# Kernel tuning notes

Hardware: AMD Instinct MI355X
Metric: run time of the kernel (lower is better)

Reference implementation:

```python
import jax, jax.numpy as jnp
import numpy as np

N, E, B = 10000, 160000, 16
IN, H, A, L, OUT = 16, 64, 8, 2, 1
MSG_IN = 2 * (H + 1) + 1   # 131 = concat(x_i, x_j, additional_message_features)
UPD_IN = H + 1 + H         # 129 = concat(x_aug, aggregated message)


def _tp(h, a, W, b):
    # scalar-irreps fully-connected O3 tensor product == bilinear map + bias
    return jnp.einsum('ni,nj,ijk->nk', h, a, W) + b


def setup_inputs() -> dict:
    key = jax.random.key(0)
    ks = jax.random.split(key, 24)
    f32 = jnp.float32
    def rn(k, shape, scale=1.0):
        return jax.random.normal(k, shape, f32) * scale
    def w(k, shape):
        fan = shape[-3] * shape[-2]
        return rn(k, shape, 1.0 / np.sqrt(fan))
    return {
        'x': rn(ks[0], (N, IN)),
        'edge_index': jax.random.randint(ks[1], (2, E), 0, N),
        'edge_attr': rn(ks[2], (E, A)),
        'node_attr': rn(ks[3], (N, A)),
        'additional_message_features': rn(ks[4], (E, 1)),
        'additional_node_features': rn(ks[5], (N, 1)),
        'batch': jnp.sort(jax.random.randint(ks[6], (N,), 0, B)),
        'W_emb': w(ks[7], (IN + 1, A, H)), 'b_emb': jnp.zeros((H,), f32),
        'Wm1': w(ks[8], (L, MSG_IN, A, H)), 'bm1': jnp.zeros((L, H), f32),
        'Wm2': w(ks[9], (L, H, A, H)), 'bm2': jnp.zeros((L, H), f32),
        'Wu1': w(ks[10], (L, UPD_IN, A, H)), 'bu1': jnp.zeros((L, H), f32),
        'Wu2': w(ks[11], (L, H, A, H)), 'bu2': jnp.zeros((L, H), f32),
        'Wp1': w(ks[12], (H, A, H)), 'bp1': jnp.zeros((H,), f32),
        'Wp2': w(ks[13], (H, A, H)), 'bp2': jnp.zeros((H,), f32),
        'Wq1': rn(ks[14], (H, H), 1.0 / np.sqrt(H)), 'bq1': jnp.zeros((H,), f32),
        'Wq2': rn(ks[15], (H, OUT), 1.0 / np.sqrt(H)), 'bq2': jnp.zeros((OUT,), f32),
    }


def _forward(x, edge_attr, node_attr, amf, anf,
             W_emb, b_emb, Wm1, bm1, Wm2, bm2, Wu1, bu1, Wu2, bu2,
             Wp1, bp1, Wp2, bp2, Wq1, bq1, Wq2, bq2, edge_index, batch):
    silu = jax.nn.silu
    src, dst = edge_index[0], edge_index[1]  # source_to_target: aggregate at dst
    n = x.shape[0]
    # embedding: concat additional node features, bilinear TP with node_attr
    h = _tp(jnp.concatenate([x, anf], -1), node_attr, W_emb, b_emb)          # [N,H]
    for l in range(Wm1.shape[0]):  # loop over structurally distinct layers
        h_aug = jnp.concatenate([h, anf], -1)                                # [N,H+1]
        m_in = jnp.concatenate([h_aug[dst], h_aug[src], amf], -1)            # [E,MSG_IN]
        m = silu(_tp(m_in, edge_attr, Wm1[l], bm1[l]))                       # TP + swish gate
        m = silu(_tp(m, edge_attr, Wm2[l], bm2[l]))                          # sg2=True -> gated too
        agg = jax.ops.segment_sum(m, dst, num_segments=n)                    # scatter-add [N,H]
        u = silu(_tp(jnp.concatenate([h_aug, agg], -1), node_attr, Wu1[l], bu1[l]))
        u = _tp(u, node_attr, Wu2[l], bu2[l])                                # no gate on 2nd TP
        h = h + u                                                            # residual, adnid stripped
    # pre-pool MLP (SwishGate TP then plain TP)
    p = silu(_tp(h, node_attr, Wp1, bp1))
    p = _tp(p, node_attr, Wp2, bp2)                                          # [N,POOL=H]
    # global mean pool over graphs
    counts = jax.ops.segment_sum(jnp.ones((n,), p.dtype), batch, num_segments=B)
    g = jax.ops.segment_sum(p, batch, num_segments=B) / jnp.maximum(counts, 1.0)[:, None]
    # post-pool: TP with trivial 1x0e attr == plain linear
    g = silu(g @ Wq1 + bq1)
    return g @ Wq2 + bq2                                                     # [B,OUT]


def reference(x, edge_index, edge_attr, node_attr, additional_message_features,
              additional_node_features, batch, W_emb, b_emb, Wm1, bm1, Wm2, bm2,
              Wu1, bu1, Wu2, bu2, Wp1, bp1, Wp2, bp2, Wq1, bq1, Wq2, bq2):
    return _forward(x, edge_attr, node_attr, additional_message_features,
                    additional_node_features, W_emb, b_emb, Wm1, bm1, Wm2, bm2,
                    Wu1, bu1, Wu2, bu2, Wp1, bp1, Wp2, bp2, Wq1, bq1, Wq2, bq2,
                    edge_index, batch)
```

## Files before the change

kernel.cpp:

```cpp
#include <hip/hip_runtime.h>
#include <hip/hip_bf16.h>
#include <math.h>

constexpr int N = 10000;
constexpr int E = 160000;
constexpr int B = 16;
constexpr int POOL_CHUNKS = 80;
constexpr int MS = 72;
constexpr int HS = 96;

typedef short bf16x8 __attribute__((ext_vector_type(8)));
typedef short bf16x4 __attribute__((ext_vector_type(4)));
typedef float f32x4 __attribute__((ext_vector_type(4)));

__device__ __forceinline__ float silu_f(float x) {
    return x / (1.0f + __expf(-x));
}
__device__ __forceinline__ float bf2f(short s) {
    union { unsigned u; float f; } c; c.u = (unsigned)(unsigned short)s << 16; return c.f;
}

__device__ __forceinline__ void w2_body(
        int idx, const float* __restrict__ Wsrc,
        __hip_bfloat16* __restrict__ Whi, __hip_bfloat16* __restrict__ Wlo) {
    int l = idx >> 15;
    int rem = idx & 32767;
    int kk = rem >> 11;
    int nt = (rem >> 9) & 3;
    int c  = (rem >> 5) & 15;
    int q  = (rem >> 3) & 3;
    int j  = rem & 7;
    int i = q * 16 + kk;
    int k = nt * 16 + c;
    float wv = Wsrc[(size_t)l * 32768 + i * 512 + j * 64 + k];
    __hip_bfloat16 hi = __float2bfloat16(wv);
    Whi[idx] = hi;
    Wlo[idx] = __float2bfloat16(wv - __bfloat162float(hi));
}

__device__ __forceinline__ void w2h_body(
        int idx, const float* __restrict__ Wsrc, __hip_bfloat16* __restrict__ Whi) {
    int l = idx >> 15;
    int rem = idx & 32767;
    int kk = rem >> 11;
    int nt = (rem >> 9) & 3;
    int c  = (rem >> 5) & 15;
    int q  = (rem >> 3) & 3;
    int j  = rem & 7;
    int i = q * 16 + kk;
    int k = nt * 16 + c;
    Whi[idx] = __float2bfloat16(Wsrc[(size_t)l * 32768 + i * 512 + j * 64 + k]);
}

__device__ __forceinline__ void wu1_body(
        int idx, const float* __restrict__ Wu1,
        __hip_bfloat16* __restrict__ Whi, __hip_bfloat16* __restrict__ Wlo) {
    int l = idx / 67584;
    int rem = idx % 67584;
    int kk = rem / 2048;
    int r2 = rem % 2048;
    int nt = (r2 >> 9) & 3;
    int c  = (r2 >> 5) & 15;
    int q  = (r2 >> 3) & 3;
    int j  = r2 & 7;
    int i = q * 33 + kk;
    float wv = (i < 129) ? Wu1[(size_t)l * 129 * 512 + i * 512 + j * 64 + nt * 16 + c] : 0.f;
    __hip_bfloat16 hi = __float2bfloat16(wv);
    Whi[idx] = hi;
    Wlo[idx] = __float2bfloat16(wv - __bfloat162float(hi));
}

__device__ __forceinline__ void wm1z_body(
        int idx, const float* __restrict__ Wm1, __hip_bfloat16* __restrict__ Whi) {
    int l = idx / 71680;
    int rem = idx % 71680;
    int kkn = rem >> 9;
    int off = rem & 511;
    int kk = kkn >> 2;
    int nt = kkn & 3;
    int c16 = off >> 5;
    int q = (off >> 3) & 3;
    int j = off & 7;
    int k = nt * 16 + c16;
    int wi = -1;
    if (kk < 17) { int i = q * 17 + kk; if (i <= 64) wi = i; }
    else if (kk < 34) { int s = q * 17 + (kk - 17); if (s <= 64) wi = 65 + s; }
    else { if (q == 0) wi = 130; }
    float wv = (wi >= 0) ? Wm1[((size_t)l * 131 + wi) * 512 + j * 64 + k] : 0.f;
    Whi[idx] = __float2bfloat16(wv);
}

constexpr int PB_W2H  = 0;
constexpr int PB_WM1Z = PB_W2H  + 256;
constexpr int PB_WU1  = PB_WM1Z + 560;
constexpr int PB_WU2  = PB_WU1  + 528;
constexpr int PB_WP1  = PB_WU2  + 256;
constexpr int PB_WP2  = PB_WP1  + 128;
constexpr int PB_ZERO = PB_WP2  + 128;
constexpr int PB_EMB  = PB_ZERO + 40;
constexpr int PB_TOTAL= PB_EMB  + 625;

__global__ __launch_bounds__(256) void k_pre(
        const float* __restrict__ Wm2, __hip_bfloat16* __restrict__ W2hi,
        const float* __restrict__ Wm1, __hip_bfloat16* __restrict__ Wm1zhi,
        const float* __restrict__ Wu1w, __hip_bfloat16* __restrict__ Wu1hi, __hip_bfloat16* __restrict__ Wu1lo,
        const float* __restrict__ Wu2w, __hip_bfloat16* __restrict__ Wu2hi, __hip_bfloat16* __restrict__ Wu2lo,
        const float* __restrict__ Wp1w, __hip_bfloat16* __restrict__ Wp1hi, __hip_bfloat16* __restrict__ Wp1lo,
        const float* __restrict__ Wp2w, __hip_bfloat16* __restrict__ Wp2hi, __hip_bfloat16* __restrict__ Wp2lo,
        int* __restrict__ hist,
        const float* __restrict__ x, const float* __restrict__ anf,
        const float* __restrict__ na, const float* __restrict__ W_emb,
        const float* __restrict__ b_emb,
        float* __restrict__ h, __hip_bfloat16* __restrict__ hb, float* __restrict__ agg) {
    __shared__ float xs[16][18];
    __shared__ float na_s[16][8];
    int tid = threadIdx.x;
    int bx = blockIdx.x;
    if (bx < PB_WM1Z) {
        w2h_body((bx - PB_W2H) * 256 + tid, Wm2, W2hi);
    } else if (bx < PB_WU1) {
        wm1z_body((bx - PB_WM1Z) * 256 + tid, Wm1, Wm1zhi);
    } else if (bx < PB_WU2) {
        wu1_body((bx - PB_WU1) * 256 + tid, Wu1w, Wu1hi, Wu1lo);
    } else if (bx < PB_WP1) {
        w2_body((bx - PB_WU2) * 256 + tid, Wu2w, Wu2hi, Wu2lo);
    } else if (bx < PB_WP2) {
        w2_body((bx - PB_WP1) * 256 + tid, Wp1w, Wp1hi, Wp1lo);
    } else if (bx < PB_ZERO) {
        w2_body((bx - PB_WP2) * 256 + tid, Wp2w, Wp2hi, Wp2lo);
    } else if (bx < PB_EMB) {
        int i = (bx - PB_ZERO) * 256 + tid;
        if (i < N) hist[i] = 0;
    } else {
        int eb = bx - PB_EMB;
        int w = tid >> 6, l = tid & 63;
        int n0 = eb * 16;
        {
            int r = tid >> 4, c = tid & 15;
            xs[r][c] = x[(size_t)(n0 + r) * 16 + c];
        }
        if (tid < 16) xs[tid][16] = anf[n0 + tid];
        if (tid < 128) na_s[tid >> 3][tid & 7] = na[(size_t)n0 * 8 + tid];
        float4 z4 = {0.f, 0.f, 0.f, 0.f};
        ((float4*)(agg + (size_t)eb * 1024))[tid] = z4;
        for (int t = tid; t < 192; t += 256)
            ((float4*)(hb + (size_t)n0 * HS))[t] = z4;
        __syncthreads();
        float acc[4];
#pragma unroll
        for (int t = 0; t < 4; ++t) acc[t] = b_emb[l];
        for (int i = 0; i < 17; ++i) {
#pragma unroll
            for (int j = 0; j < 8; ++j) {
                float wv = W_emb[(i * 8 + j) * 64 + l];
#pragma unroll
                for (int t = 0; t < 4; ++t) {
                    int nn = w * 4 + t;
                    acc[t] = fmaf(xs[nn][i] * na_s[nn][j], wv, acc[t]);
                }
            }
        }
        int slot = (l / 17) * 24 + l % 17;
#pragma unroll
        for (int t = 0; t < 4; ++t) {
            int n = n0 + w * 4 + t;
            h[(size_t)n * 64 + l] = acc[t];
            hb[(size_t)n * HS + slot] = __float2bfloat16(acc[t]);
        }
        if (tid < 16) hb[(size_t)(n0 + tid) * HS + 85] = __float2bfloat16(xs[tid][16]);
    }
}

__global__ __launch_bounds__(256) void k_hist(
        const int* __restrict__ eidx, int* __restrict__ hist) {
    int e = blockIdx.x * 256 + threadIdx.x;
    if (e < E) atomicAdd(&hist[eidx[E + e]], 1);
}

__global__ __launch_bounds__(1024) void k_scan(
        const int* __restrict__ hist, int* __restrict__ cursor) {
    __shared__ int wsum[16];
    int t = threadIdx.x;
    int base = t * 10;
    int loc[10];
    int s = 0;
#pragma unroll
    for (int i = 0; i < 10; ++i) {
        int v = (base + i < N) ? hist[base + i] : 0;
        loc[i] = s;
        s += v;
    }
    int lane = t & 63, w = t >> 6;
    int incl = s;
    for (int off = 1; off < 64; off <<= 1) {
        int u = __shfl_up(incl, off, 64);
        if (lane >= off) incl += u;
    }
    if (lane == 63) wsum[w] = incl;
    __syncthreads();
    if (t == 0) {
        int a = 0;
        for (int i2 = 0; i2 < 16; ++i2) { int v = wsum[i2]; wsum[i2] = a; a += v; }
    }
    __syncthreads();
    int excl = incl - s + wsum[w];
#pragma unroll
    for (int i = 0; i < 10; ++i) {
        int p = base + i;
        if (p < N) cursor[p] = excl + loc[i];
    }
}

__global__ __launch_bounds__(256) void k_scatter_sort(
        const int* __restrict__ eidx, const float* __restrict__ ea,
        const float* __restrict__ amf, int* __restrict__ cursor,
        int* __restrict__ srcS, int* __restrict__ dstS,
        float* __restrict__ amfS, float* __restrict__ eaS) {
    int e = blockIdx.x * 256 + threadIdx.x;
    if (e < E) {
        int d = eidx[E + e];
        int p = atomicAdd(&cursor[d], 1);
        srcS[p] = eidx[e];
        dstS[p] = d;
        amfS[p] = amf[e];
        float4 a0 = ((const float4*)ea)[(size_t)e * 2];
        float4 a1 = ((const float4*)ea)[(size_t)e * 2 + 1];
        ((float4*)eaS)[(size_t)p * 2] = a0;
        ((float4*)eaS)[(size_t)p * 2 + 1] = a1;
    }
}

__device__ __forceinline__ void zgemm_stage(
        const __hip_bfloat16* xsrc, int xstride, int kkmax, int Lq,
        int w, int c16, int q, int lofs, const float* naA,
        const __hip_bfloat16* __restrict__ Whi, const __hip_bfloat16* __restrict__ Wlo,
        float (*part_s)[16][64]) {
    f32x4 zero4 = {0.f, 0.f, 0.f, 0.f};
    f32x4 acc[4];
#pragma unroll
    for (int nt = 0; nt < 4; ++nt) acc[nt] = zero4;
    for (int kk = w; kk < kkmax; kk += 4) {
        bf16x8 bh[4], bl[4];
#pragma unroll
        for (int nt = 0; nt < 4; ++nt) {
            int off = (kk * 4 + nt) * 512 + lofs;
            bh[nt] = *(const bf16x8*)(Whi + off);
            bl[nt] = *(const bf16x8*)(Wlo + off);
        }
        float mv = __bfloat162float(xsrc[c16 * xstride + q * Lq + kk]);
        union { bf16x8 v; __hip_bfloat16 hx[8]; } au;
#pragma unroll
        for (int j = 0; j < 8; ++j) au.hx[j] = __float2bfloat16(mv * naA[j]);
#pragma unroll
        for (int nt = 0; nt < 4; ++nt) {
            acc[nt] = __builtin_amdgcn_mfma_f32_16x16x32_bf16(au.v, bh[nt], acc[nt], 0, 0, 0);
            acc[nt] = __builtin_amdgcn_mfma_f32_16x16x32_bf16(au.v, bl[nt], acc[nt], 0, 0, 0);
        }
    }
#pragma unroll
    for (int nt = 0; nt < 4; ++nt)
#pragma unroll
        for (int r = 0; r < 4; ++r) part_s[w][q * 4 + r][nt * 16 + c16] = acc[nt][r];
}

__global__ __launch_bounds__(256, 4) void k_edge(
        const int* __restrict__ srcS, const int* __restrict__ dstS,
        const float* __restrict__ amfS, const float* __restrict__ eaS,
        const __hip_bfloat16* __restrict__ hb,
        const __hip_bfloat16* __restrict__ W1hi, const float* __restrict__ bm1_l,
        const __hip_bfloat16* __restrict__ W2hi,
        const float* __restrict__ bm2_l, float* __restrict__ agg) {
    __shared__ __align__(16) char smem_u[128 * 66 * 4];
    __shared__ int dst_s[128];
    __hip_bfloat16* m_s = (__hip_bfloat16*)smem_u;
    float* m2 = (float*)smem_u;

    int tid = threadIdx.x;
    int l = tid & 63, w = tid >> 6;
    int e0 = blockIdx.x * 128;
    if (tid < 128) dst_s[tid] = dstS[e0 + tid];

    int c16 = l & 15, q = l >> 4;
    int e0w = w * 32;
    float eaA[2][8], amfA[2];
    int dL[2], sL[2];
#pragma unroll
    for (int mt = 0; mt < 2; ++mt) {
        int e = e0 + e0w + mt * 16 + c16;
        float4 a0 = ((const float4*)eaS)[(size_t)e * 2];
        float4 a1 = ((const float4*)eaS)[(size_t)e * 2 + 1];
        eaA[mt][0] = a0.x; eaA[mt][1] = a0.y; eaA[mt][2] = a0.z; eaA[mt][3] = a0.w;
        eaA[mt][4] = a1.x; eaA[mt][5] = a1.y; eaA[mt][6] = a1.z; eaA[mt][7] = a1.w;
        amfA[mt] = amfS[e];
        dL[mt] = dstS[e];
        sL[mt] = srcS[e];
    }
    float bR1[4], bR2[4];
#pragma unroll
    for (int nt = 0; nt < 4; ++nt) {
        bR1[nt] = bm1_l[nt * 16 + c16];
        bR2[nt] = bm2_l[nt * 16 + c16];
    }
    int lofs = (c16 * 4 + q) * 8;
    f32x4 zero4 = {0.f, 0.f, 0.f, 0.f};

    bf16x4 xD[2][5], xS[2][5];
#pragma unroll
    for (int mt = 0; mt < 2; ++mt) {
        const __hip_bfloat16* bd = hb + (size_t)dL[mt] * HS + q * 24;
        const __hip_bfloat16* bs = hb + (size_t)sL[mt] * HS + q * 24;
#pragma unroll
        for (int t = 0; t < 5; ++t) {
            xD[mt][t] = *(const bf16x4*)(bd + t * 4);
            xS[mt][t] = *(const bf16x4*)(bs + t * 4);
        }
    }

    f32x4 acc1[2][4];
#pragma unroll
    for (int mt = 0; mt < 2; ++mt)
#pragma unroll
        for (int nt = 0; nt < 4; ++nt) acc1[mt][nt] = zero4;
#pragma unroll
    for (int kk = 0; kk < 17; ++kk) {
        bf16x8 bh[4];
#pragma unroll
        for (int nt = 0; nt < 4; ++nt)
            bh[nt] = *(const bf16x8*)(W1hi + (kk * 4 + nt) * 512 + lofs);
#pragma unroll
        for (int mt = 0; mt < 2; ++mt) {
            float xv = bf2f(xD[mt][kk >> 2][kk & 3]);
            union { bf16x8 v; __hip_bfloat16 hx[8]; } au;
#pragma unroll
            for (int j = 0; j < 8; ++j) au.hx[j] = __float2bfloat16(xv * eaA[mt][j]);
#pragma unroll
            for (int nt = 0; nt < 4; ++nt)
                acc1[mt][nt] = __builtin_amdgcn_mfma_f32_16x16x32_bf16(au.v, bh[nt], acc1[mt][nt], 0, 0, 0);
        }
    }
#pragma unroll
    for (int kk = 0; kk < 17; ++kk) {
        bf16x8 bh[4];
#pragma unroll
        for (int nt = 0; nt < 4; ++nt)
            bh[nt] = *(const bf16x8*)(W1hi + ((17 + kk) * 4 + nt) * 512 + lofs);
#pragma unroll
        for (int mt = 0; mt < 2; ++mt) {
            float xv = bf2f(xS[mt][kk >> 2][kk & 3]);
            union { bf16x8 v; __hip_bfloat16 hx[8]; } au;
#pragma unroll
            for (int j = 0; j < 8; ++j) au.hx[j] = __float2bfloat16(xv * eaA[mt][j]);
#pragma unroll
            for (int nt = 0; nt < 4; ++nt)
                acc1[mt][nt] = __builtin_amdgcn_mfma_f32_16x16x32_bf16(au.v, bh[nt], acc1[mt][nt], 0, 0, 0);
        }
    }
    {
        bf16x8 bh[4];
#pragma unroll
        for (int nt = 0; nt < 4; ++nt)
            bh[nt] = *(const bf16x8*)(W1hi + (34 * 4 + nt) * 512 + lofs);
#pragma unroll
        for (int mt = 0; mt < 2; ++mt) {
            float xv = (q == 0) ? amfA[mt] : 0.f;
            union { bf16x8 v; __hip_bfloat16 hx[8]; } au;
#pragma unroll
            for (int j = 0; j < 8; ++j) au.hx[j] = __float2bfloat16(xv * eaA[mt][j]);
#pragma unroll
            for (int nt = 0; nt < 4; ++nt)
                acc1[mt][nt] = __builtin_amdgcn_mfma_f32_16x16x32_bf16(au.v, bh[nt], acc1[mt][nt], 0, 0, 0);
        }
    }
#pragma unroll
    for (int mt = 0; mt < 2; ++mt)
#pragma unroll
        for (int nt = 0; nt < 4; ++nt) {
            int kd = nt * 16 + c16;
            float bias = bR1[nt];
#pragma unroll
            for (int r = 0; r < 4; ++r) {
                int e = e0w + mt * 16 + q * 4 + r;
                m_s[e * MS + kd] = __float2bfloat16(silu_f(bias + acc1[mt][nt][r]));
            }
        }

    bf16x4 mR[2][4];
#pragma unroll
    for (int mt = 0; mt < 2; ++mt)
#pragma unroll
        for (int t = 0; t < 4; ++t)
            mR[mt][t] = *(const bf16x4*)&m_s[(e0w + mt * 16 + c16) * MS + q * 16 + t * 4];

    __syncthreads();

    f32x4 acc[2][4];
#pragma unroll
    for (int mt = 0; mt < 2; ++mt)
#pragma unroll
        for (int nt = 0; nt < 4; ++nt) acc[mt][nt] = zero4;
#pragma unroll
    for (int kk = 0; kk < 16; ++kk) {
        bf16x8 bh[4];
#pragma unroll
        for (int nt = 0; nt < 4; ++nt)
            bh[nt] = *(const bf16x8*)(W2hi + (kk * 4 + nt) * 512 + lofs);
#pragma unroll
        for (int mt = 0; mt < 2; ++mt) {
            float mv = bf2f(mR[mt][kk >> 2][kk & 3]);
            union { bf16x8 v; __hip_bfloat16 h[8]; } au;
#pragma unroll
            for (int j = 0; j < 8; ++j) au.h[j] = __float2bfloat16(mv * eaA[mt][j]);
#pragma unroll
            for (int nt = 0; nt < 4; ++nt)
                acc[mt][nt] = __builtin_amdgcn_mfma_f32_16x16x32_bf16(au.v, bh[nt], acc[mt][nt], 0, 0, 0);
        }
    }
#pragma unroll
    for (int mt = 0; mt < 2; ++mt)
#pragma unroll
        for (int nt = 0; nt < 4; ++nt) {
            int kd = nt * 16 + c16;
            float bias = bR2[nt];
#pragma unroll
            for (int r = 0; r < 4; ++r) {
                int e = e0w + mt * 16 + q * 4 + r;
                m2[e * 66 + kd] = silu_f(bias + acc[mt][nt][r]);
            }
        }

    {
        int r0 = w * 32;
        float run = 0.f;
        int cur_d = dst_s[r0];
        for (int e = r0; e < r0 + 32; ++e) {
            int d = dst_s[e];
            if (d != cur_d) {
                atomicAdd(&agg[(size_t)cur_d * 64 + l], run);
                run = 0.f;
                cur_d = d;
            }
            run += m2[e * 66 + l];
        }
        atomicAdd(&agg[(size_t)cur_d * 64 + l], run);
    }
}

__global__ __launch_bounds__(256) void k_upd_hb(
        const float* __restrict__ h_in, const float* __restrict__ anf,
        const float* __restrict__ na, const float* __restrict__ agg_in,
        const __hip_bfloat16* __restrict__ W1hi, const __hip_bfloat16* __restrict__ W1lo,
        const float* __restrict__ bu1_l,
        const __hip_bfloat16* __restrict__ W2hi_, const __hip_bfloat16* __restrict__ W2lo_,
        const float* __restrict__ bu2_l,
        float* __restrict__ h, __hip_bfloat16* __restrict__ hb, float* __restrict__ agg) {
    __shared__ __align__(16) __hip_bfloat16 xa_s[16 * 136];
    __shared__ __align__(16) __hip_bfloat16 u1_s[16 * 72];
    __shared__ float part_s[4][16][64];
    int tid = threadIdx.x;
    int w = tid >> 6, l = tid & 63;
    int n0 = blockIdx.x * 16;
    for (int idx = tid; idx < 16 * 132; idx += 256) {
        int r = idx / 132, c = idx % 132;
        int n = n0 + r;
        float v;
        if (c < 64) v = h_in[(size_t)n * 64 + c];
        else if (c == 64) v = anf[n];
        else if (c < 129) v = agg_in[(size_t)n * 64 + (c - 65)];
        else v = 0.f;
        xa_s[r * 136 + c] = __float2bfloat16(v);
    }
    int c16 = l & 15, q = l >> 4;
    float naA[8];
#pragma unroll
    for (int j = 0; j < 8; ++j) naA[j] = na[(size_t)(n0 + c16) * 8 + j];
    __syncthreads();
    float4 z4 = {0.f, 0.f, 0.f, 0.f};
    ((float4*)(agg + (size_t)blockIdx.x * 1024))[tid] = z4;
    for (int t = tid; t < 192; t += 256)
        ((float4*)(hb + (size_t)n0 * HS))[t] = z4;
    int lofs = (c16 * 4 + q) * 8;
    zgemm_stage(xa_s, 136, 33, 33, w, c16, q, lofs, naA, W1hi, W1lo, part_s);
    __syncthreads();
    for (int t = tid; t < 1024; t += 256) {
        int row = t >> 6, col = t & 63;
        float v = part_s[0][row][col] + part_s[1][row][col] + part_s[2][row][col] +
                  part_s[3][row][col] + bu1_l[col];
        u1_s[row * 72 + col] = __float2bfloat16(silu_f(v));
    }
    __syncthreads();
    zgemm_stage(u1_s, 72, 16, 16, w, c16, q, lofs, naA, W2hi_, W2lo_, part_s);
    __syncthreads();
    for (int t = tid; t < 1024; t += 256) {
        int row = t >> 6, col = t & 63;
        float v = part_s[0][row][col] + part_s[1][row][col] + part_s[2][row][col] +
                  part_s[3][row][col] + bu2_l[col];
        int n = n0 + row;
        float hn = h[(size_t)n * 64 + col] + v;
        h[(size_t)n * 64 + col] = hn;
        hb[(size_t)n * HS + (col / 17) * 24 + col % 17] = __float2bfloat16(hn);
    }
    if (tid < 16) hb[(size_t)(n0 + tid) * HS + 85] = __float2bfloat16(anf[n0 + tid]);
}

__global__ __launch_bounds__(256) void k_upd_prepool(
        const float* __restrict__ h_in, const float* __restrict__ anf,
        const float* __restrict__ na, const float* __restrict__ agg_in,
        const __hip_bfloat16* __restrict__ W1hi, const __hip_bfloat16* __restrict__ W1lo,
        const float* __restrict__ bu1_l,
        const __hip_bfloat16* __restrict__ W2hi_, const __hip_bfloat16* __restrict__ W2lo_,
        const float* __restrict__ bu2_l,
        const __hip_bfloat16* __restrict__ Wp1hi, const __hip_bfloat16* __restrict__ Wp1lo,
        const float* __restrict__ bp1,
        const __hip_bfloat16* __restrict__ Wp2hi, const __hip_bfloat16* __restrict__ Wp2lo,
        const float* __restrict__ bp2,
        float* __restrict__ p2) {
    __shared__ __align__(16) __hip_bfloat16 xa_s[16 * 136];
    __shared__ __align__(16) __hip_bfloat16 u1_s[16 * 72];
    __shared__ __align__(16) __hip_bfloat16 x2_s[16 * 72];
    __shared__ float part_s[4][16][64];
    int tid = threadIdx.x;
    int w = tid >> 6, l = tid & 63;
    int n0 = blockIdx.x * 16;
    for (int idx = tid; idx < 16 * 132; idx += 256) {
        int r = idx / 132, c = idx % 132;
        int n = n0 + r;
        float v;
        if (c < 64) v = h_in[(size_t)n * 64 + c];
        else if (c == 64) v = anf[n];
        else if (c < 129) v = agg_in[(size_t)n * 64 + (c - 65)];
        else v = 0.f;
        xa_s[r * 136 + c] = __float2bfloat16(v);
    }
    int c16 = l & 15, q = l >> 4;
    float naA[8];
#pragma unroll
    for (int j = 0; j < 8; ++j) naA[j] = na[(size_t)(n0 + c16) * 8 + j];
    __syncthreads();
    int lofs = (c16 * 4 + q) * 8;
    zgemm_stage(xa_s, 136, 33, 33, w, c16, q, lofs, naA, W1hi, W1lo, part_s);
    __syncthreads();
    for (int t = tid; t < 1024; t += 256) {
        int row = t >> 6, col = t & 63;
        float v = part_s[0][row][col] + part_s[1][row][col] + part_s[2][row][col] +
                  part_s[3][row][col] + bu1_l[col];
        u1_s[row * 72 + col] = __float2bfloat16(silu_f(v));
    }
    __syncthreads();
    zgemm_stage(u1_s, 72, 16, 16, w, c16, q, lofs, naA, W2hi_, W2lo_, part_s);
    __syncthreads();
    for (int t = tid; t < 1024; t += 256) {
        int row = t >> 6, col = t & 63;
        float v = part_s[0][row][col] + part_s[1][row][col] + part_s[2][row][col] +
                  part_s[3][row][col] + bu2_l[col];
        float hn = h_in[(size_t)(n0 + row) * 64 + col] + v;
        x2_s[row * 72 + col] = __float2bfloat16(hn);
    }
    __syncthreads();
    zgemm_stage(x2_s, 72, 16, 16, w, c16, q, lofs, naA, Wp1hi, Wp1lo, part_s);
    __syncthreads();
    for (int t = tid; t < 1024; t += 256) {
        int row = t >> 6, col = t & 63;
        float v = part_s[0][row][col] + part_s[1][row][col] + part_s[2][row][col] +
                  part_s[3][row][col] + bp1[col];
        u1_s[row * 72 + col] = __float2bfloat16(silu_f(v));
    }
    __syncthreads();
    zgemm_stage(u1_s, 72, 16, 16, w, c16, q, lofs, naA, Wp2hi, Wp2lo, part_s);
    __syncthreads();
    for (int t = tid; t < 1024; t += 256) {
        int row = t >> 6, col = t & 63;
        float v = part_s[0][row][col] + part_s[1][row][col] + part_s[2][row][col] +
                  part_s[3][row][col] + bp2[col];
        p2[(size_t)(n0 + row) * 64 + col] = v;
    }
}

__global__ __launch_bounds__(256) void k_pool(
        const float* __restrict__ p2, const int* __restrict__ batch,
        float* __restrict__ partial_p, float* __restrict__ partial_cnt) {
    __shared__ float acc_s[16 * 64];
    __shared__ float cnt_s[16];
    int tid = threadIdx.x;
    for (int idx = tid; idx < 1024; idx += 256) acc_s[idx] = 0.f;
    if (tid < 16) cnt_s[tid] = 0.f;
    __syncthreads();
    int w = tid >> 6, k = tid & 63;
    int base = blockIdx.x * 125;
    for (int i = 0; i < 32; ++i) {
        int nl = i * 4 + w;
        if (nl < 125) {
            int n = base + nl;
            int b = batch[n];
            atomicAdd(&acc_s[b * 64 + k], p2[(size_t)n * 64 + k]);
            if (k == 0) atomicAdd(&cnt_s[b], 1.0f);
        }
    }
    __syncthreads();
    for (int idx = tid; idx < 1024; idx += 256)
        partial_p[(size_t)blockIdx.x * 1024 + idx] = acc_s[idx];
    if (tid < 16) partial_cnt[blockIdx.x * 16 + tid] = cnt_s[tid];
}

__global__ __launch_bounds__(1024) void k_final(
        const float* __restrict__ partial_p, const float* __restrict__ partial_cnt,
        const float* __restrict__ Wq1, const float* __restrict__ bq1,
        const float* __restrict__ Wq2, const float* __restrict__ bq2,
        float* __restrict__ out) {
    __shared__ float g[16][64];
    int b = threadIdx.x >> 6, k = threadIdx.x & 63;
    float s = 0.f, cc = 0.f;
    for (int c = 0; c < POOL_CHUNKS; ++c) s += partial_p[(size_t)c * 1024 + b * 64 + k];
    for (int c = 0; c < POOL_CHUNKS; ++c) cc += partial_cnt[c * 16 + b];
    g[b][k] = s / fmaxf(cc, 1.0f);
    __syncthreads();
    float acc = bq1[k];
#pragma unroll
    for (int i = 0; i < 64; ++i) acc = fmaf(g[b][i], Wq1[i * 64 + k], acc);
    float v = silu_f(acc) * Wq2[k];
#pragma unroll
    for (int off = 32; off > 0; off >>= 1) v += __shfl_down(v, off, 64);
    if (k == 0) out[b] = v + bq2[0];
}

extern "C" void kernel_launch(void* const* d_in, const int* in_sizes, int n_in,
                              void* d_out, int out_size, void* d_ws, size_t ws_size,
                              hipStream_t stream) {
    const float* x    = (const float*)d_in[0];
    const int*   eidx = (const int*)  d_in[1];
    const float* ea   = (const float*)d_in[2];
    const float* na   = (const float*)d_in[3];
    const float* amf  = (const float*)d_in[4];
    const float* anf  = (const float*)d_in[5];
    const int*   batch= (const int*)  d_in[6];
    const float* W_emb= (const float*)d_in[7];
    const float* b_emb= (const float*)d_in[8];
    const float* Wm1  = (const float*)d_in[9];
    const float* bm1  = (const float*)d_in[10];
    const float* Wm2  = (const float*)d_in[11];
    const float* bm2  = (const float*)d_in[12];
    const float* Wu1  = (const float*)d_in[13];
    const float* bu1  = (const float*)d_in[14];
    const float* Wu2  = (const float*)d_in[15];
    const float* bu2  = (const float*)d_in[16];
    const float* Wp1  = (const float*)d_in[17];
    const float* bp1  = (const float*)d_in[18];
    const float* Wp2  = (const float*)d_in[19];
    const float* bp2  = (const float*)d_in[20];
    const float* Wq1  = (const float*)d_in[21];
    const float* bq1  = (const float*)d_in[22];
    const float* Wq2  = (const float*)d_in[23];
    const float* bq2  = (const float*)d_in[24];

    float* ws = (float*)d_ws;
    float* h      = ws;
    float* agg    = h + (size_t)N * 64;
    float* p2     = agg + (size_t)N * 64;
    float* part_p = p2 + (size_t)N * 64;
    float* part_c = part_p + POOL_CHUNKS * 1024;
    float* fend   = part_c + POOL_CHUNKS * 16;
    __hip_bfloat16* hb     = (__hip_bfloat16*)fend;
    __hip_bfloat16* W2hi   = hb + (size_t)N * HS;
    __hip_bfloat16* Wm1zhi = W2hi + 65536;
    __hip_bfloat16* Wu1hi  = Wm1zhi + 143360;
    __hip_bfloat16* Wu1lo  = Wu1hi + 135168;
    __hip_bfloat16* Wu2hi  = Wu1lo + 135168;
    __hip_bfloat16* Wu2lo  = Wu2hi + 65536;
    __hip_bfloat16* Wp1hi  = Wu2lo + 65536;
    __hip_bfloat16* Wp1lo  = Wp1hi + 32768;
    __hip_bfloat16* Wp2hi  = Wp1lo + 32768;
    __hip_bfloat16* Wp2lo  = Wp2hi + 32768;
    int* hist   = (int*)(Wp2lo + 32768);
    int* cursor = hist + N;
    int* srcS   = cursor + N;
    int* dstS   = srcS + E;
    float* amfS = (float*)(dstS + E);
    float* eaS  = amfS + E;

    k_pre<<<PB_TOTAL, 256, 0, stream>>>(
        Wm2, W2hi, Wm1, Wm1zhi, Wu1, Wu1hi, Wu1lo, Wu2, Wu2hi, Wu2lo,
        Wp1, Wp1hi, Wp1lo, Wp2, Wp2hi, Wp2lo, hist,
        x, anf, na, W_emb, b_emb, h, hb, agg);

    k_hist<<<(E + 255) / 256, 256, 0, stream>>>(eidx, hist);
    k_scan<<<1, 1024, 0, stream>>>(hist, cursor);
    k_scatter_sort<<<(E + 255) / 256, 256, 0, stream>>>(eidx, ea, amf, cursor,
                                                        srcS, dstS, amfS, eaS);

    k_edge<<<E / 128, 256, 0, stream>>>(srcS, dstS, amfS, eaS, hb,
                                        Wm1zhi, bm1, W2hi, bm2, agg);
    k_upd_hb<<<625, 256, 0, stream>>>(h, anf, na, agg,
                                      Wu1hi, Wu1lo, bu1,
                                      Wu2hi, Wu2lo, bu2,
                                      h, hb, agg);
    k_edge<<<E / 128, 256, 0, stream>>>(srcS, dstS, amfS, eaS, hb,
                                        Wm1zhi + 71680, bm1 + 64,
                                        W2hi + 32768, bm2 + 64, agg);
    k_upd_prepool<<<625, 256, 0, stream>>>(h, anf, na, agg,
                                           Wu1hi + 67584, Wu1lo + 67584, bu1 + 64,
                                           Wu2hi + 32768, Wu2lo + 32768, bu2 + 64,
                                           Wp1hi, Wp1lo, bp1, Wp2hi, Wp2lo, bp2, p2);
    k_pool<<<POOL_CHUNKS, 256, 0, stream>>>(p2, batch, part_p, part_c);
    k_final<<<1, 1024, 0, stream>>>(part_p, part_c, Wq1, bq1, Wq2, bq2, (float*)d_out);
}
```

Baseline: 385.8 us.

## Pack edge records, shrink per-wave edge LDS and drop block barrier

Scatter-sort now writes src, amf and edge attributes together as one interleaved 48-byte record per edge instead of into separate arrays, so the edge kernel fetches them with three float4 loads. The edge kernel gives each wave its own 4.6KB LDS slice, processes the segmented reduction in 16-edge halves, and swaps the block-wide __syncthreads for a compiler barrier. It also raises the launch-bounds occupancy hint from 4 to 8 blocks. The aim is to cut LDS footprint and synchronization so more waves stay resident, at the risk of register spilling under the tighter bound and of relying on wave-local LDS ordering for correctness.

Result: slower. 1.376 ms (+256.6%).

```diff
diff --git a/kernel.cpp b/kernel.cpp
--- a/kernel.cpp
+++ b/kernel.cpp
@@ -214,19 +214,20 @@
 __global__ __launch_bounds__(256) void k_scatter_sort(
         const int* __restrict__ eidx, const float* __restrict__ ea,
         const float* __restrict__ amf, int* __restrict__ cursor,
-        int* __restrict__ srcS, int* __restrict__ dstS,
-        float* __restrict__ amfS, float* __restrict__ eaS) {
+        int* __restrict__ dstS, float4* __restrict__ recs) {
     int e = blockIdx.x * 256 + threadIdx.x;
     if (e < E) {
         int d = eidx[E + e];
         int p = atomicAdd(&cursor[d], 1);
-        srcS[p] = eidx[e];
         dstS[p] = d;
-        amfS[p] = amf[e];
         float4 a0 = ((const float4*)ea)[(size_t)e * 2];
         float4 a1 = ((const float4*)ea)[(size_t)e * 2 + 1];
-        ((float4*)eaS)[(size_t)p * 2] = a0;
-        ((float4*)eaS)[(size_t)p * 2 + 1] = a1;
+        float4 r0 = {__int_as_float(eidx[e]), amf[e], a0.x, a0.y};
+        float4 r1 = {a0.z, a0.w, a1.x, a1.y};
+        float4 r2 = {a1.z, a1.w, 0.f, 0.f};
+        recs[(size_t)p * 3 + 0] = r0;
+        recs[(size_t)p * 3 + 1] = r1;
+        recs[(size_t)p * 3 + 2] = r2;
     }
 }
 
@@ -263,22 +264,21 @@
         for (int r = 0; r < 4; ++r) part_s[w][q * 4 + r][nt * 16 + c16] = acc[nt][r];
 }
 
-__global__ __launch_bounds__(256, 4) void k_edge(
-        const int* __restrict__ srcS, const int* __restrict__ dstS,
-        const float* __restrict__ amfS, const float* __restrict__ eaS,
+__global__ __launch_bounds__(256, 8) void k_edge(
+        const float4* __restrict__ recs, const int* __restrict__ dstS,
         const __hip_bfloat16* __restrict__ hb,
         const __hip_bfloat16* __restrict__ W1hi, const float* __restrict__ bm1_l,
         const __hip_bfloat16* __restrict__ W2hi,
         const float* __restrict__ bm2_l, float* __restrict__ agg) {
-    __shared__ __align__(16) char smem_u[128 * 66 * 4];
+    __shared__ __align__(16) char smem_u[4 * 4608];
     __shared__ int dst_s[128];
-    __hip_bfloat16* m_s = (__hip_bfloat16*)smem_u;
-    float* m2 = (float*)smem_u;
-
     int tid = threadIdx.x;
     int l = tid & 63, w = tid >> 6;
     int e0 = blockIdx.x * 128;
-    if (tid < 128) dst_s[tid] = dstS[e0 + tid];
+    __hip_bfloat16* m_s = (__hip_bfloat16*)(smem_u + w * 4608);
+    float* m2 = (float*)(smem_u + w * 4608);
+
+    if (l < 32) dst_s[w * 32 + l] = dstS[e0 + w * 32 + l];
 
     int c16 = l & 15, q = l >> 4;
     int e0w = w * 32;
@@ -287,13 +287,15 @@
 #pragma unroll
     for (int mt = 0; mt < 2; ++mt) {
         int e = e0 + e0w + mt * 16 + c16;
-        float4 a0 = ((const float4*)eaS)[(size_t)e * 2];
-        float4 a1 = ((const float4*)eaS)[(size_t)e * 2 + 1];
-        eaA[mt][0] = a0.x; eaA[mt][1] = a0.y; eaA[mt][2] = a0.z; eaA[mt][3] = a0.w;
-        eaA[mt][4] = a1.x; eaA[mt][5] = a1.y; eaA[mt][6] = a1.z; eaA[mt][7] = a1.w;
-        amfA[mt] = amfS[e];
+        float4 r0 = recs[(size_t)e * 3];
+        float4 r1 = recs[(size_t)e * 3 + 1];
+        float4 r2 = recs[(size_t)e * 3 + 2];
+        sL[mt] = __float_as_int(r0.x);
+        amfA[mt] = r0.y;
+        eaA[mt][0] = r0.z; eaA[mt][1] = r0.w;
+        eaA[mt][2] = r1.x; eaA[mt][3] = r1.y; eaA[mt][4] = r1.z; eaA[mt][5] = r1.w;
+        eaA[mt][6] = r2.x; eaA[mt][7] = r2.y;
         dL[mt] = dstS[e];
-        sL[mt] = srcS[e];
     }
     float bR1[4], bR2[4];
 #pragma unroll
@@ -379,8 +381,8 @@
             float bias = bR1[nt];
 #pragma unroll
             for (int r = 0; r < 4; ++r) {
-                int e = e0w + mt * 16 + q * 4 + r;
-                m_s[e * MS + kd] = __float2bfloat16(silu_f(bias + acc1[mt][nt][r]));
+                int el = mt * 16 + q * 4 + r;
+                m_s[el * MS + kd] = __float2bfloat16(silu_f(bias + acc1[mt][nt][r]));
             }
         }
 
@@ -389,9 +391,9 @@
     for (int mt = 0; mt < 2; ++mt)
 #pragma unroll
         for (int t = 0; t < 4; ++t)
-            mR[mt][t] = *(const bf16x4*)&m_s[(e0w + mt * 16 + c16) * MS + q * 16 + t * 4];
-
-    __syncthreads();
+            mR[mt][t] = *(const bf16x4*)&m_s[(mt * 16 + c16) * MS + q * 16 + t * 4];
+
+    asm volatile("" ::: "memory");
 
     f32x4 acc[2][4];
 #pragma unroll
@@ -415,33 +417,31 @@
                 acc[mt][nt] = __builtin_amdgcn_mfma_f32_16x16x32_bf16(au.v, bh[nt], acc[mt][nt], 0, 0, 0);
         }
     }
-#pragma unroll
-    for (int mt = 0; mt < 2; ++mt)
+
+#pragma unroll
+    for (int mt = 0; mt < 2; ++mt) {
 #pragma unroll
         for (int nt = 0; nt < 4; ++nt) {
             int kd = nt * 16 + c16;
             float bias = bR2[nt];
 #pragma unroll
-            for (int r = 0; r < 4; ++r) {
-                int e = e0w + mt * 16 + q * 4 + r;
-                m2[e * 66 + kd] = silu_f(bias + acc[mt][nt][r]);
-            }
-        }
-
-    {
-        int r0 = w * 32;
+            for (int r = 0; r < 4; ++r)
+                m2[(q * 4 + r) * 66 + kd] = silu_f(bias + acc[mt][nt][r]);
+        }
+        int rb = w * 32 + mt * 16;
         float run = 0.f;
-        int cur_d = dst_s[r0];
-        for (int e = r0; e < r0 + 32; ++e) {
-            int d = dst_s[e];
+        int cur_d = dst_s[rb];
+        for (int i = 0; i < 16; ++i) {
+            int d = dst_s[rb + i];
             if (d != cur_d) {
                 atomicAdd(&agg[(size_t)cur_d * 64 + l], run);
                 run = 0.f;
                 cur_d = d;
             }
-            run += m2[e * 66 + l];
+            run += m2[i * 66 + l];
         }
         atomicAdd(&agg[(size_t)cur_d * 64 + l], run);
+        asm volatile("" ::: "memory");
     }
 }
 
@@ -671,10 +671,8 @@
     __hip_bfloat16* Wp2lo  = Wp2hi + 32768;
     int* hist   = (int*)(Wp2lo + 32768);
     int* cursor = hist + N;
-    int* srcS   = cursor + N;
-    int* dstS   = srcS + E;
-    float* amfS = (float*)(dstS + E);
-    float* eaS  = amfS + E;
+    int* dstS   = cursor + N;
+    float4* recs = (float4*)(dstS + E);
 
     k_pre<<<PB_TOTAL, 256, 0, stream>>>(
         Wm2, W2hi, Wm1, Wm1zhi, Wu1, Wu1hi, Wu1lo, Wu2, Wu2hi, Wu2lo,
@@ -683,16 +681,15 @@
 
     k_hist<<<(E + 255) / 256, 256, 0, stream>>>(eidx, hist);
     k_scan<<<1, 1024, 0, stream>>>(hist, cursor);
-    k_scatter_sort<<<(E + 255) / 256, 256, 0, stream>>>(eidx, ea, amf, cursor,
-                                                        srcS, dstS, amfS, eaS);
-
-    k_edge<<<E / 128, 256, 0, stream>>>(srcS, dstS, amfS, eaS, hb,
+    k_scatter_sort<<<(E + 255) / 256, 256, 0, stream>>>(eidx, ea, amf, cursor, dstS, recs);
+
+    k_edge<<<E / 128, 256, 0, stream>>>(recs, dstS, hb,
                                         Wm1zhi, bm1, W2hi, bm2, agg);
     k_upd_hb<<<625, 256, 0, stream>>>(h, anf, na, agg,
                                       Wu1hi, Wu1lo, bu1,
                                       Wu2hi, Wu2lo, bu2,
                                       h, hb, agg);
-    k_edge<<<E / 128, 256, 0, stream>>>(srcS, dstS, amfS, eaS, hb,
+    k_edge<<<E / 128, 256, 0, stream>>>(recs, dstS, hb,
                                         Wm1zhi + 71680, bm1 + 64,
                                         W2hi + 32768, bm2 + 64, agg);
     k_upd_prepool<<<625, 256, 0, stream>>>(h, anf, na, agg,
```
